# Kernel optimization log

Hardware: AMD Instinct MI355X
Metric: run time of the kernel (lower is better)

## Reference

```python
import jax, jax.numpy as jnp
import numpy as np

LOOKBACK = 1
LOOKAHEAD = 0
SEQ, BATCH, IN, HID = 1024, 16, 1024, 1024
K = LOOKBACK + 1 + LOOKAHEAD


def quick_gelu(x):
    return x * jax.nn.sigmoid(1.702 * x)


def setup_inputs() -> dict:
    key = jax.random.key(0)
    ks = jax.random.split(key, 5)
    scale = 1.0 / np.sqrt(IN * K)  # like torch Conv1d default init scale
    X = jax.random.normal(ks[0], (SEQ, BATCH, IN), dtype=jnp.float32)
    Wz = jax.random.normal(ks[1], (HID, IN, K), dtype=jnp.float32) * scale
    bz = jax.random.normal(ks[2], (HID,), dtype=jnp.float32) * scale
    Wf = jax.random.normal(ks[3], (HID, IN, K), dtype=jnp.float32) * scale
    bf = jax.random.normal(ks[4], (HID,), dtype=jnp.float32) * scale
    return {"X": X, "Wz": Wz, "bz": bz, "Wf": Wf, "bf": bf}


def _conv1d(x_pad, W, b):
    # x_pad: (B, Cin, T+K-1), W: (Cout, Cin, K) -> (B, Cout, T)
    y = jax.lax.conv_general_dilated(
        x_pad, W, window_strides=(1,), padding="VALID",
        dimension_numbers=("NCH", "OIH", "NCH"))
    return y + b[None, :, None]


def reference(X, Wz, bz, Wf, bf):
    # pad time dim: lookback zeros before, lookahead zeros after
    X_pad = jnp.pad(X, ((LOOKBACK, LOOKAHEAD), (0, 0), (0, 0)))
    X_pad = jnp.transpose(X_pad, (1, 2, 0))  # (B, Cin, T+K-1)
    Z = jnp.transpose(_conv1d(X_pad, Wz, bz), (2, 0, 1))  # (T, B, H)
    F = jnp.transpose(_conv1d(X_pad, Wf, bf), (2, 0, 1))  # (T, B, H)
    Z = quick_gelu(Z)
    F = jax.nn.sigmoid(F)

    def step(h, fz):
        f, z = fz
        h = f * z + (1.0 - f) * h
        return h, h

    h0 = jnp.zeros((BATCH, HID), dtype=X.dtype)
    _, H = jax.lax.scan(step, h0, (F, Z))  # H: (T, B, HID)
    return H, H[-1:, :, :]
```

## Files before the change

### kernel.cpp

```cpp
#include <hip/hip_runtime.h>
#include <stdint.h>

#define T_SEQ 1024
#define B_SZ  16
#define C_IN  1024
#define C_HID 1024
#define M_ROWS (T_SEQ * B_SZ)
#define N_COLS (2 * C_HID)
#define K_DIM  (2 * C_IN)

#define NCHUNK 64
#define CLEN   (T_SEQ / NCHUNK)
#define NBH    (B_SZ * C_HID)

typedef __attribute__((ext_vector_type(8))) short bf16x8;
typedef __attribute__((ext_vector_type(4))) float f32x4;
typedef unsigned short u16;

#define MFMA __builtin_amdgcn_mfma_f32_16x16x32_bf16

__device__ __forceinline__ u16 f2bf(float f) {
  union { float f; unsigned u; } v; v.f = f;
  unsigned r = v.u + 0x7fffu + ((v.u >> 16) & 1u);
  return (u16)(r >> 16);
}
__device__ __forceinline__ float bf2f(unsigned s) {
  union { unsigned u; float f; } v; v.u = s << 16;
  return v.f;
}

__device__ __forceinline__ void async_cp16(const u16* g, u16* l) {
  __builtin_amdgcn_global_load_lds(
      (const __attribute__((address_space(1))) unsigned*)(uintptr_t)g,
      (__attribute__((address_space(3))) unsigned*)(uintptr_t)l,
      16, 0, 0);
}

__global__ __launch_bounds__(256) void k_prep(const float* __restrict__ X,
                                              const float* __restrict__ Wz,
                                              const float* __restrict__ Wf,
                                              u16* __restrict__ Xp,
                                              u16* __restrict__ Wt) {
  int blk = blockIdx.x;
  if (blk < 16400) {
    int i = blk * 256 + threadIdx.x;
    const int total4 = (M_ROWS + B_SZ) * C_IN / 4;
    if (i >= total4) return;
    int e = i << 2;
    const int PAD = B_SZ * C_IN;
    ushort4 o;
    if (e < PAD) {
      o.x = o.y = o.z = o.w = 0;
    } else {
      float4 v = *reinterpret_cast<const float4*>(X + (e - PAD));
      o.x = f2bf(v.x); o.y = f2bf(v.y); o.z = f2bf(v.z); o.w = f2bf(v.w);
    }
    *reinterpret_cast<ushort4*>(Xp + e) = o;
  } else {
    int i = (blk - 16400) * 256 + threadIdx.x;
    if (i >= 2 * 1024 * 1024) return;
    int g  = i >> 20;
    int hc = i & ((1 << 20) - 1);
    int h  = hc >> 10;
    int c  = hc & 1023;
    const float* W = g ? Wf : Wz;
    float2 w = *reinterpret_cast<const float2*>(W + ((size_t)(h << 10) + c) * 2);
    size_t n = ((size_t)h << 1) | (size_t)g;
    Wt[n * K_DIM + c]        = f2bf(w.x);
    Wt[n * K_DIM + 1024 + c] = f2bf(w.y);
  }
}

__global__ __launch_bounds__(512, 2) void k_gemm8(const u16* __restrict__ Xp,
                                                  const u16* __restrict__ Wt,
                                                  const float* __restrict__ bz,
                                                  const float* __restrict__ bfv,
                                                  u16* __restrict__ Cb) {
  __shared__ u16 lds[2][2][2][8192];
  const int tid  = threadIdx.x;
  const int lane = tid & 63;
  const int wid  = tid >> 6;
  const int wr = wid >> 2;
  const int wc = wid & 3;
  const int lr = lane & 15;

  int wg = (blockIdx.x & 7) * 64 + (blockIdx.x >> 3);
  const int m0 = (wg >> 3) << 8;
  const int n0 = (wg & 7) << 8;

  const int p    = tid << 4;
  const int q    = p ^ (((p >> 7) & 7) << 4);
  const int grow = q >> 7;
  const int gcol = (q & 127) >> 1;
  const int ldsw = (tid >> 6) << 9;

  const int rbase = lr << 6;
  int co[2];
#pragma unroll
  for (int ks = 0; ks < 2; ++ks)
    co[ks] = ((((ks << 6) | ((lane >> 4) << 4)) ^ ((lr & 7) << 4)) >> 1);

  auto stage = [&](int j) {
    int kt = j >> 2, part = j & 3, buf = kt & 1;
    if (part >= 2) {
      int h = part - 2;
      const u16* g = Xp + (size_t)(m0 + (h << 7) + grow + ((kt >= 16) ? B_SZ : 0)) * C_IN
                        + ((kt & 15) << 6) + gcol;
      u16* l = &lds[buf][0][h][ldsw];
      async_cp16(g, l);
      async_cp16(g + (size_t)64 * C_IN, l + 4096);
    } else {
      const u16* g = Wt + (size_t)(n0 + (part << 7) + grow) * K_DIM + (kt << 6) + gcol;
      u16* l = &lds[buf][1][part][ldsw];
      async_cp16(g, l);
      async_cp16(g + (size_t)64 * K_DIM, l + 4096);
    }
  };

  f32x4 acc[8][4] = {};
  bf16x8 a[4][2], b0[2][2], b1[2][2];

  for (int j = 0; j < 7; ++j) stage(j);
  asm volatile("s_waitcnt vmcnt(6)" ::: "memory");
  __builtin_amdgcn_s_barrier();

#pragma unroll 2
  for (int t = 0; t < 32; ++t) {
    const int buf = t & 1;
    const u16* pA = &lds[buf][0][wr][0];
    const u16* pB = &lds[buf][1][wc >> 1][(wc & 1) << 12];
    const int jb = 4 * t + 7;

#pragma unroll
    for (int mi = 0; mi < 4; ++mi)
#pragma unroll
      for (int ks = 0; ks < 2; ++ks)
        a[mi][ks] = *(const bf16x8*)(pA + (mi << 10) + rbase + co[ks]);
#pragma unroll
    for (int ni = 0; ni < 2; ++ni)
#pragma unroll
      for (int ks = 0; ks < 2; ++ks)
        b0[ni][ks] = *(const bf16x8*)(pB + (ni << 10) + rbase + co[ks]);
    if (jb < 128) stage(jb);
    __builtin_amdgcn_s_barrier();
    asm volatile("s_waitcnt lgkmcnt(0)" ::: "memory");
    __builtin_amdgcn_s_setprio(1);
#pragma unroll
    for (int mi = 0; mi < 4; ++mi)
#pragma unroll
      for (int ni = 0; ni < 2; ++ni)
#pragma unroll
        for (int ks = 0; ks < 2; ++ks)
          acc[mi][ni] = MFMA(a[mi][ks], b0[ni][ks], acc[mi][ni], 0, 0, 0);
    __builtin_amdgcn_s_setprio(0);
    __builtin_amdgcn_s_barrier();

#pragma unroll
    for (int ni = 0; ni < 2; ++ni)
#pragma unroll
      for (int ks = 0; ks < 2; ++ks)
        b1[ni][ks] = *(const bf16x8*)(pB + ((2 + ni) << 10) + rbase + co[ks]);
    if (jb + 1 < 128) stage(jb + 1);
    __builtin_amdgcn_s_barrier();
    asm volatile("s_waitcnt lgkmcnt(0)" ::: "memory");
    __builtin_amdgcn_s_setprio(1);
#pragma unroll
    for (int mi = 0; mi < 4; ++mi)
#pragma unroll
      for (int ni = 0; ni < 2; ++ni)
#pragma unroll
        for (int ks = 0; ks < 2; ++ks)
          acc[mi][2 + ni] = MFMA(a[mi][ks], b1[ni][ks], acc[mi][2 + ni], 0, 0, 0);
    __builtin_amdgcn_s_setprio(0);
    __builtin_amdgcn_s_barrier();

#pragma unroll
    for (int mi = 0; mi < 4; ++mi)
#pragma unroll
      for (int ks = 0; ks < 2; ++ks)
        a[mi][ks] = *(const bf16x8*)(pA + ((4 + mi) << 10) + rbase + co[ks]);
    if (jb + 2 < 128) stage(jb + 2);
    __builtin_amdgcn_s_barrier();
    asm volatile("s_waitcnt lgkmcnt(0)" ::: "memory");
    __builtin_amdgcn_s_setprio(1);
#pragma unroll
    for (int mi = 0; mi < 4; ++mi)
#pragma unroll
      for (int ni = 0; ni < 2; ++ni)
#pragma unroll
        for (int ks = 0; ks < 2; ++ks)
          acc[4 + mi][2 + ni] = MFMA(a[mi][ks], b1[ni][ks], acc[4 + mi][2 + ni], 0, 0, 0);
    __builtin_amdgcn_s_setprio(0);
    __builtin_amdgcn_s_barrier();

    if (jb + 3 < 128) stage(jb + 3);
    if (t < 30) asm volatile("s_waitcnt vmcnt(6)" ::: "memory");
    else        asm volatile("s_waitcnt vmcnt(0)" ::: "memory");
    __builtin_amdgcn_s_barrier();
    __builtin_amdgcn_s_setprio(1);
#pragma unroll
    for (int mi = 0; mi < 4; ++mi)
#pragma unroll
      for (int ni = 0; ni < 2; ++ni)
#pragma unroll
        for (int ks = 0; ks < 2; ++ks)
          acc[4 + mi][ni] = MFMA(a[mi][ks], b0[ni][ks], acc[4 + mi][ni], 0, 0, 0);
    __builtin_amdgcn_s_setprio(0);
    __builtin_amdgcn_s_barrier();
  }

  const int colp = lane & 15;
  const bool isz = (colp & 1) == 0;
  const float kk = isz ? 1.702f : 1.0f;
  const int hbase = (n0 + (wc << 6) + colp) >> 1;
  const int fmb = (m0 >> 4) + (wr << 3);
  const int fnb = (n0 >> 4) + (wc << 2);
#pragma unroll
  for (int ni = 0; ni < 4; ++ni) {
    float bias = isz ? bz[hbase + 8 * ni] : bfv[hbase + 8 * ni];
#pragma unroll
    for (int mi = 0; mi < 8; ++mi) {
      ushort4 o;
#pragma unroll
      for (int r = 0; r < 4; ++r) {
        float v = acc[mi][ni][r] + bias;
        float s = 1.f / (1.f + __expf(-kk * v));
        ((u16*)&o)[r] = f2bf(isz ? v * s : s);
      }
      size_t fi = (size_t)(fmb + mi) * 128 + (fnb + ni);
      *reinterpret_cast<ushort4*>(Cb + fi * 256 + (lane << 2)) = o;
    }
  }
}

__global__ __launch_bounds__(256) void k_scan1(const u16* __restrict__ Cb,
                                               float* __restrict__ Ap,
                                               float* __restrict__ Bp) {
  int i = blockIdx.x * 256 + threadIdx.x;
  int h  = i & (C_HID - 1);
  int b4 = (i >> 10) & 3;
  int c  = i >> 12;
  const size_t lane_off = (size_t)(h >> 3) * 256 + b4 * 64 + (h & 7) * 8;
  float hh[4] = {0.f, 0.f, 0.f, 0.f}, P[4] = {1.f, 1.f, 1.f, 1.f};
#pragma unroll 8
  for (int tt = 0; tt < CLEN; ++tt) {
    size_t t = (size_t)c * CLEN + tt;
    uint4 v = *reinterpret_cast<const uint4*>(Cb + t * 32768 + lane_off);
    float z[4] = {bf2f(v.x & 0xffffu), bf2f(v.x >> 16),
                  bf2f(v.y & 0xffffu), bf2f(v.y >> 16)};
    float f[4] = {bf2f(v.z & 0xffffu), bf2f(v.z >> 16),
                  bf2f(v.w & 0xffffu), bf2f(v.w >> 16)};
#pragma unroll
    for (int r = 0; r < 4; ++r) {
      hh[r] += f[r] * (z[r] - hh[r]);
      P[r]  *= (1.f - f[r]);
    }
  }
  *reinterpret_cast<f32x4*>(Ap + (size_t)i * 4) = (f32x4){hh[0], hh[1], hh[2], hh[3]};
  *reinterpret_cast<f32x4*>(Bp + (size_t)i * 4) = (f32x4){P[0], P[1], P[2], P[3]};
}

__global__ __launch_bounds__(256) void k_scan3(const u16* __restrict__ Cb,
                                               const float* __restrict__ Ap,
                                               const float* __restrict__ Bp,
                                               float* __restrict__ out) {
  int i = blockIdx.x * 256 + threadIdx.x;
  int h  = i & (C_HID - 1);
  int b4 = (i >> 10) & 3;
  int c  = i >> 12;
  int j  = i & 4095;
  float hh[4] = {0.f, 0.f, 0.f, 0.f};
  for (int cc = 0; cc < c; ++cc) {
    size_t idx = ((size_t)cc * 4096 + j) * 4;
    f32x4 A = *reinterpret_cast<const f32x4*>(Ap + idx);
    f32x4 B = *reinterpret_cast<const f32x4*>(Bp + idx);
#pragma unroll
    for (int r = 0; r < 4; ++r) hh[r] = A[r] + B[r] * hh[r];
  }
  const size_t lane_off = (size_t)(h >> 3) * 256 + b4 * 64 + (h & 7) * 8;
#pragma unroll 8
  for (int tt = 0; tt < CLEN; ++tt) {
    size_t t = (size_t)c * CLEN + tt;
    uint4 v = *reinterpret_cast<const uint4*>(Cb + t * 32768 + lane_off);
    float z[4] = {bf2f(v.x & 0xffffu), bf2f(v.x >> 16),
                  bf2f(v.y & 0xffffu), bf2f(v.y >> 16)};
    float f[4] = {bf2f(v.z & 0xffffu), bf2f(v.z >> 16),
                  bf2f(v.w & 0xffffu), bf2f(v.w >> 16)};
    float* op = out + t * 16384 + (size_t)b4 * 4096 + h;
#pragma unroll
    for (int r = 0; r < 4; ++r) {
      hh[r] += f[r] * (z[r] - hh[r]);
      op[r * 1024] = hh[r];
    }
  }
  if (c == NCHUNK - 1) {
    float* tp = out + (size_t)M_ROWS * C_HID + (size_t)b4 * 4096 + h;
#pragma unroll
    for (int r = 0; r < 4; ++r) tp[r * 1024] = hh[r];
  }
}

extern "C" void kernel_launch(void* const* d_in, const int* in_sizes, int n_in,
                              void* d_out, int out_size, void* d_ws, size_t ws_size,
                              hipStream_t stream) {
  const float* X   = (const float*)d_in[0];
  const float* Wz  = (const float*)d_in[1];
  const float* bz  = (const float*)d_in[2];
  const float* Wf  = (const float*)d_in[3];
  const float* bf_ = (const float*)d_in[4];
  float* out = (float*)d_out;

  u16* Xp = (u16*)d_ws;
  u16* Wt = Xp + (size_t)(M_ROWS + B_SZ) * C_IN;
  u16* Cb = Wt + (size_t)N_COLS * K_DIM;
  float* Ap = (float*)Xp;
  float* Bp = Ap + (size_t)NCHUNK * NBH;

  hipLaunchKernelGGL(k_prep, dim3(16400 + 8192), dim3(256), 0, stream,
                     X, Wz, Wf, Xp, Wt);
  hipLaunchKernelGGL(k_gemm8, dim3((M_ROWS / 256) * (N_COLS / 256)), dim3(512), 0,
                     stream, Xp, Wt, bz, bf_, Cb);
  hipLaunchKernelGGL(k_scan1, dim3(NCHUNK * 4096 / 256), dim3(256), 0, stream,
                     Cb, Ap, Bp);
  hipLaunchKernelGGL(k_scan3, dim3(NCHUNK * 4096 / 256), dim3(256), 0, stream,
                     Cb, Ap, Bp, out);
}
```

Measured before the change: 299.9 us.

## Fuse per-chunk scan into GEMM epilogue and merge scan kernels

The GEMM epilogue now pairs z/f columns via lane shuffles and runs the local recurrence over each 256-row tile (16 timesteps). It uses an LDS exchange between the two wave rows to stitch the halves, and stores the affine transform (h, P) in bf16 instead of the activations. The two scan kernels are replaced by one kernel that composes prior chunks' final transforms and applies them per timestep. This removes a full pass over the intermediate and the Ap/Bp buffers. It costs an extra barrier and registers in the epilogue, and adds bf16 rounding on accumulated h and P, which may hurt accuracy.

After: 297.4 us. No clear change (-0.8%).

```diff
diff --git a/kernel.cpp b/kernel.cpp
--- a/kernel.cpp
+++ b/kernel.cpp
@@ -212,91 +212,106 @@
   const int colp = lane & 15;
   const bool isz = (colp & 1) == 0;
   const float kk = isz ? 1.702f : 1.0f;
-  const int hbase = (n0 + (wc << 6) + colp) >> 1;
-  const int fmb = (m0 >> 4) + (wr << 3);
-  const int fnb = (n0 >> 4) + (wc << 2);
+  const int jj = colp >> 1;
+  const int b4 = lane >> 4;
+  const int hbase = ((n0 + (wc << 6)) >> 1) + jj;
+  const int c    = m0 >> 8;
+  const int nfb  = (n0 >> 4) + (wc << 2);
+  float* exA = (float*)&lds[0][0][0][0];
+  float* exB = exA + 2048;
+
+  uint4 trj[8];
 #pragma unroll
   for (int ni = 0; ni < 4; ++ni) {
     float bias = isz ? bz[hbase + 8 * ni] : bfv[hbase + 8 * ni];
+    float hh[4] = {0.f, 0.f, 0.f, 0.f}, P[4] = {1.f, 1.f, 1.f, 1.f};
 #pragma unroll
     for (int mi = 0; mi < 8; ++mi) {
-      ushort4 o;
+      unsigned tw[4];
 #pragma unroll
       for (int r = 0; r < 4; ++r) {
         float v = acc[mi][ni][r] + bias;
         float s = 1.f / (1.f + __expf(-kk * v));
-        ((u16*)&o)[r] = f2bf(isz ? v * s : s);
+        float act = isz ? v * s : s;
+        float par = __shfl_xor(act, 1, 64);
+        float z = isz ? act : par;
+        float f = isz ? par : act;
+        hh[r] += f * (z - hh[r]);
+        P[r]  *= (1.f - f);
+        tw[r] = (unsigned)f2bf(hh[r]) | ((unsigned)f2bf(P[r]) << 16);
       }
-      size_t fi = (size_t)(fmb + mi) * 128 + (fnb + ni);
-      *reinterpret_cast<ushort4*>(Cb + fi * 256 + (lane << 2)) = o;
-    }
-  }
-}
-
-__global__ __launch_bounds__(256) void k_scan1(const u16* __restrict__ Cb,
-                                               float* __restrict__ Ap,
-                                               float* __restrict__ Bp) {
+      if (wr == 0) {
+        if (!(lane & 1)) {
+          size_t fi = (size_t)((c << 4) + mi) * 128 + nfb + ni;
+          uint4 o; o.x = tw[0]; o.y = tw[1]; o.z = tw[2]; o.w = tw[3];
+          *reinterpret_cast<uint4*>(Cb + fi * 256 + (b4 << 6) + (jj << 3)) = o;
+        }
+      } else {
+        uint4 o; o.x = tw[0]; o.y = tw[1]; o.z = tw[2]; o.w = tw[3];
+        trj[mi] = o;
+      }
+    }
+    const int xi = (((((wc << 2) | b4) << 3) | jj) << 2 | ni) << 2;
+    if (wr == 0 && !(lane & 1)) {
+#pragma unroll
+      for (int r = 0; r < 4; ++r) { exA[xi + r] = hh[r]; exB[xi + r] = P[r]; }
+    }
+    __syncthreads();
+    if (wr == 1 && !(lane & 1)) {
+      float A0[4], B0[4];
+#pragma unroll
+      for (int r = 0; r < 4; ++r) { A0[r] = exA[xi + r]; B0[r] = exB[xi + r]; }
+#pragma unroll
+      for (int mi = 0; mi < 8; ++mi) {
+        uint4 o;
+        unsigned* ow = &o.x;
+        const unsigned* iw = &trj[mi].x;
+#pragma unroll
+        for (int r = 0; r < 4; ++r) {
+          float hp = bf2f(iw[r] & 0xffffu);
+          float pp = bf2f(iw[r] >> 16);
+          float H2 = hp + pp * A0[r];
+          float P2 = pp * B0[r];
+          ow[r] = (unsigned)f2bf(H2) | ((unsigned)f2bf(P2) << 16);
+        }
+        size_t fi = (size_t)((c << 4) + 8 + mi) * 128 + nfb + ni;
+        *reinterpret_cast<uint4*>(Cb + fi * 256 + (b4 << 6) + (jj << 3)) = o;
+      }
+    }
+  }
+}
+
+__global__ __launch_bounds__(256) void k_scan(const u16* __restrict__ Cb,
+                                              float* __restrict__ out) {
   int i = blockIdx.x * 256 + threadIdx.x;
   int h  = i & (C_HID - 1);
   int b4 = (i >> 10) & 3;
   int c  = i >> 12;
   const size_t lane_off = (size_t)(h >> 3) * 256 + b4 * 64 + (h & 7) * 8;
-  float hh[4] = {0.f, 0.f, 0.f, 0.f}, P[4] = {1.f, 1.f, 1.f, 1.f};
-#pragma unroll 8
+  float hh[4] = {0.f, 0.f, 0.f, 0.f};
+  for (int cc = 0; cc < c; ++cc) {
+    uint4 w = *reinterpret_cast<const uint4*>(
+        Cb + ((size_t)cc * CLEN + CLEN - 1) * 32768 + lane_off);
+    const unsigned* ww = &w.x;
+#pragma unroll
+    for (int r = 0; r < 4; ++r) {
+      float A = bf2f(ww[r] & 0xffffu), B = bf2f(ww[r] >> 16);
+      hh[r] = A + B * hh[r];
+    }
+  }
+#pragma unroll 4
   for (int tt = 0; tt < CLEN; ++tt) {
     size_t t = (size_t)c * CLEN + tt;
-    uint4 v = *reinterpret_cast<const uint4*>(Cb + t * 32768 + lane_off);
-    float z[4] = {bf2f(v.x & 0xffffu), bf2f(v.x >> 16),
-                  bf2f(v.y & 0xffffu), bf2f(v.y >> 16)};
-    float f[4] = {bf2f(v.z & 0xffffu), bf2f(v.z >> 16),
-                  bf2f(v.w & 0xffffu), bf2f(v.w >> 16)};
+    uint4 w = *reinterpret_cast<const uint4*>(Cb + t * 32768 + lane_off);
+    const unsigned* ww = &w.x;
+    float* op = out + t * 16384 + (size_t)b4 * 4096 + h;
 #pragma unroll
     for (int r = 0; r < 4; ++r) {
-      hh[r] += f[r] * (z[r] - hh[r]);
-      P[r]  *= (1.f - f[r]);
-    }
-  }
-  *reinterpret_cast<f32x4*>(Ap + (size_t)i * 4) = (f32x4){hh[0], hh[1], hh[2], hh[3]};
-  *reinterpret_cast<f32x4*>(Bp + (size_t)i * 4) = (f32x4){P[0], P[1], P[2], P[3]};
-}
-
-__global__ __launch_bounds__(256) void k_scan3(const u16* __restrict__ Cb,
-                                               const float* __restrict__ Ap,
-                                               const float* __restrict__ Bp,
-                                               float* __restrict__ out) {
-  int i = blockIdx.x * 256 + threadIdx.x;
-  int h  = i & (C_HID - 1);
-  int b4 = (i >> 10) & 3;
-  int c  = i >> 12;
-  int j  = i & 4095;
-  float hh[4] = {0.f, 0.f, 0.f, 0.f};
-  for (int cc = 0; cc < c; ++cc) {
-    size_t idx = ((size_t)cc * 4096 + j) * 4;
-    f32x4 A = *reinterpret_cast<const f32x4*>(Ap + idx);
-    f32x4 B = *reinterpret_cast<const f32x4*>(Bp + idx);
-#pragma unroll
-    for (int r = 0; r < 4; ++r) hh[r] = A[r] + B[r] * hh[r];
-  }
-  const size_t lane_off = (size_t)(h >> 3) * 256 + b4 * 64 + (h & 7) * 8;
-#pragma unroll 8
-  for (int tt = 0; tt < CLEN; ++tt) {
-    size_t t = (size_t)c * CLEN + tt;
-    uint4 v = *reinterpret_cast<const uint4*>(Cb + t * 32768 + lane_off);
-    float z[4] = {bf2f(v.x & 0xffffu), bf2f(v.x >> 16),
-                  bf2f(v.y & 0xffffu), bf2f(v.y >> 16)};
-    float f[4] = {bf2f(v.z & 0xffffu), bf2f(v.z >> 16),
-                  bf2f(v.w & 0xffffu), bf2f(v.w >> 16)};
-    float* op = out + t * 16384 + (size_t)b4 * 4096 + h;
-#pragma unroll
-    for (int r = 0; r < 4; ++r) {
-      hh[r] += f[r] * (z[r] - hh[r]);
-      op[r * 1024] = hh[r];
-    }
-  }
-  if (c == NCHUNK - 1) {
-    float* tp = out + (size_t)M_ROWS * C_HID + (size_t)b4 * 4096 + h;
-#pragma unroll
-    for (int r = 0; r < 4; ++r) tp[r * 1024] = hh[r];
+      float v = bf2f(ww[r] & 0xffffu) + bf2f(ww[r] >> 16) * hh[r];
+      op[r * 1024] = v;
+      if (c == NCHUNK - 1 && tt == CLEN - 1)
+        out[(size_t)M_ROWS * C_HID + (size_t)b4 * 4096 + h + r * 1024] = v;
+    }
   }
 }
 
@@ -313,15 +328,11 @@
   u16* Xp = (u16*)d_ws;
   u16* Wt = Xp + (size_t)(M_ROWS + B_SZ) * C_IN;
   u16* Cb = Wt + (size_t)N_COLS * K_DIM;
-  float* Ap = (float*)Xp;
-  float* Bp = Ap + (size_t)NCHUNK * NBH;
 
   hipLaunchKernelGGL(k_prep, dim3(16400 + 8192), dim3(256), 0, stream,
                      X, Wz, Wf, Xp, Wt);
   hipLaunchKernelGGL(k_gemm8, dim3((M_ROWS / 256) * (N_COLS / 256)), dim3(512), 0,
                      stream, Xp, Wt, bz, bf_, Cb);
-  hipLaunchKernelGGL(k_scan1, dim3(NCHUNK * 4096 / 256), dim3(256), 0, stream,
-                     Cb, Ap, Bp);
-  hipLaunchKernelGGL(k_scan3, dim3(NCHUNK * 4096 / 256), dim3(256), 0, stream,
-                     Cb, Ap, Bp, out);
-}
+  hipLaunchKernelGGL(k_scan, dim3(NCHUNK * 4096 / 256), dim3(256), 0, stream,
+                     Cb, out);
+}
```
